# Kernel optimization log

Hardware: AMD Instinct MI355X
Metric: run time of the kernel (lower is better)

## Reference

```python
import jax, jax.numpy as jnp
import numpy as np

THRESHOLD = 1.0


def heaviside(x):
    return (x > 0).astype(x.dtype)


def lif_parallel(x, W_ih, b_ih, b_hh, beta):
    """snntorch LeakyParallel: RNN with relu nonlinearity and diagonal
    recurrent weight = beta, followed by threshold spike (no reset).
    x: [T, B, I]; W_ih: [H, I]; beta: [H]. Returns spikes [T, B, H]."""
    beta = jnp.clip(beta, 0.0, 1.0)
    # input projection is time-parallel (one big GEMM)
    z = jnp.einsum('tbi,hi->tbh', x, W_ih) + b_ih + b_hh  # [T, B, H]

    def step(h, z_t):
        h_new = jax.nn.relu(z_t + beta * h)
        return h_new, h_new

    h0 = jnp.zeros(z.shape[1:], z.dtype)
    _, mem = jax.lax.scan(step, h0, z)  # [T, B, H]
    return heaviside(mem - THRESHOLD)


def setup_inputs() -> dict:
    key = jax.random.key(0)
    ks = jax.random.split(key, 9)
    T, B, I, H, O = 200, 256, 784, 1000, 10
    s1 = 1.0 / np.sqrt(I)
    s2 = 1.0 / np.sqrt(H)
    return {
        'x': jax.random.normal(ks[0], (T, B, I), dtype=jnp.float32),
        'W_ih1': jax.random.normal(ks[1], (H, I), dtype=jnp.float32) * s1,
        'b_ih1': jax.random.normal(ks[2], (H,), dtype=jnp.float32) * s1,
        'b_hh1': jax.random.normal(ks[3], (H,), dtype=jnp.float32) * s1,
        'beta1': jnp.full((H,), 0.95, dtype=jnp.float32),
        'W_ih2': jax.random.normal(ks[4], (O, H), dtype=jnp.float32) * s2,
        'b_ih2': jax.random.normal(ks[5], (O,), dtype=jnp.float32) * s2,
        'b_hh2': jax.random.normal(ks[6], (O,), dtype=jnp.float32) * s2,
        'beta2': jnp.full((O,), 0.95, dtype=jnp.float32),
    }


def reference(x, W_ih1, b_ih1, b_hh1, beta1, W_ih2, b_ih2, b_hh2, beta2):
    spk1 = lif_parallel(x, W_ih1, b_ih1, b_hh1, beta1)   # [T, B, 1000]
    spk2 = lif_parallel(spk1, W_ih2, b_ih2, b_hh2, beta2)  # [T, B, 10]
    return spk2
```

## Files before the change

kernel.cpp:

```cpp
#include <hip/hip_runtime.h>
#include <cstdint>
#include <cstddef>

#define T_STEPS 200
#define B_SZ    256
#define I_SZ    784
#define H_SZ    1000
#define O_SZ    10
#define M_ROWS  (T_STEPS * B_SZ)

#define KT        25
#define TILE_WORDS 4096
#define MBLKS     400
#define NBLKS     8

__device__ __forceinline__ int swz32(int g) { return (g & 24) | ((g + (g >> 3)) & 7); }
__device__ __forceinline__ int inv32(int p) { return (p & 24) | ((p - (p >> 3)) & 7); }

typedef const __attribute__((address_space(1))) void gvoid;
typedef __attribute__((address_space(3))) void lvoid;
__device__ __forceinline__ void gload16(const void* g, void* l) {
    __builtin_amdgcn_global_load_lds((gvoid*)g, (lvoid*)l, 16, 0, 0);
}

__global__ __launch_bounds__(256) void pack_kernel(
    const float* __restrict__ src, float* __restrict__ dst, int nrows)
{
    int bid = blockIdx.x;
    int blk = bid / KT, kt = bid - blk * KT;

    __shared__ float T[32 * 132];
    const int tid = threadIdx.x;

    #pragma unroll
    for (int it = 0; it < 4; ++it) {
        int id = tid + it * 256;
        int r  = id >> 3;
        int c4 = id & 7;
        int row = blk * 128 + r;
        int k   = kt * 32 + c4 * 4;
        float4 v = make_float4(0.f, 0.f, 0.f, 0.f);
        if (row < nrows && k < I_SZ)
            v = *(const float4*)(src + (size_t)row * I_SZ + k);
        T[(c4*4 + 0) * 132 + r] = v.x;
        T[(c4*4 + 1) * 132 + r] = v.y;
        T[(c4*4 + 2) * 132 + r] = v.z;
        T[(c4*4 + 3) * 132 + r] = v.w;
    }
    __syncthreads();

    float* out = dst + (size_t)(blk * KT + kt) * TILE_WORDS;
    #pragma unroll
    for (int it = 0; it < 4; ++it) {
        int id = tid + it * 256;
        int k  = id >> 5;
        int pg = id & 31;
        int g  = inv32(pg);
        float4 v = *(const float4*)&T[k * 132 + g * 4];
        *(float4*)(out + k * 128 + pg * 4) = v;
    }
}

__global__ __launch_bounds__(256, 4) void gemm1_v3(
    const float* __restrict__ Xp, const float* __restrict__ Wp,
    const float* __restrict__ b_ih, const float* __restrict__ b_hh,
    float* __restrict__ Z)
{
    __shared__ float Al[TILE_WORDS];
    __shared__ float Bl[TILE_WORDS];

    const int tid = threadIdx.x;
    const int tr  = tid >> 4;
    const int tc  = tid & 15;

    int bid  = blockIdx.x;
    int wg   = (bid & 7) * 400 + (bid >> 3);
    int mblk = wg >> 3;
    int nblk = wg & 7;
    const int row0 = mblk * 128;
    const int col0 = nblk * 128;

    const int a0 = swz32(2*tr)     * 4;
    const int a1 = swz32(2*tr + 1) * 4;
    const int b0 = swz32(2*tc)     * 4;
    const int b1 = swz32(2*tc + 1) * 4;

    const float* pA = Xp + (size_t)mblk * KT * TILE_WORDS;
    const float* pB = Wp + (size_t)nblk * KT * TILE_WORDS;

    float acc[8][8] = {};

    for (int kt = 0; kt < KT; ++kt) {
        const float* sA = pA + kt * TILE_WORDS + tid * 4;
        const float* sB = pB + kt * TILE_WORDS + tid * 4;
        gload16(sA,        &Al[        tid * 4]);
        gload16(sA + 1024, &Al[1024 + tid * 4]);
        gload16(sA + 2048, &Al[2048 + tid * 4]);
        gload16(sA + 3072, &Al[3072 + tid * 4]);
        gload16(sB,        &Bl[        tid * 4]);
        gload16(sB + 1024, &Bl[1024 + tid * 4]);
        gload16(sB + 2048, &Bl[2048 + tid * 4]);
        gload16(sB + 3072, &Bl[3072 + tid * 4]);
        __syncthreads();

        #pragma unroll 2
        for (int k = 0; k < 32; ++k) {
            const int kb = k * 128;
            float4 A0 = *(const float4*)&Al[kb + a0];
            float4 A1 = *(const float4*)&Al[kb + a1];
            float4 B0 = *(const float4*)&Bl[kb + b0];
            float4 B1 = *(const float4*)&Bl[kb + b1];
            float a[8] = {A0.x, A0.y, A0.z, A0.w, A1.x, A1.y, A1.z, A1.w};
            float b[8] = {B0.x, B0.y, B0.z, B0.w, B1.x, B1.y, B1.z, B1.w};
            #pragma unroll
            for (int i = 0; i < 8; ++i)
                #pragma unroll
                for (int j = 0; j < 8; ++j)
                    acc[i][j] = fmaf(a[i], b[j], acc[i][j]);
        }
        __syncthreads();
    }

    float bias[8];
    #pragma unroll
    for (int j = 0; j < 8; ++j) {
        int cc = col0 + tc * 8 + j;
        bias[j] = (cc < H_SZ) ? (b_ih[cc] + b_hh[cc]) : 0.f;
    }

    const bool full = (col0 + 127 < H_SZ);
    #pragma unroll
    for (int i = 0; i < 8; ++i) {
        int rr = row0 + tr * 8 + i;
        float* zrow = Z + (size_t)rr * H_SZ + col0 + tc * 8;
        if (full) {
            float4 v0 = make_float4(acc[i][0] + bias[0], acc[i][1] + bias[1],
                                    acc[i][2] + bias[2], acc[i][3] + bias[3]);
            float4 v1 = make_float4(acc[i][4] + bias[4], acc[i][5] + bias[5],
                                    acc[i][6] + bias[6], acc[i][7] + bias[7]);
            *(float4*)(zrow + 0) = v0;
            *(float4*)(zrow + 4) = v1;
        } else {
            #pragma unroll
            for (int j = 0; j < 8; ++j) {
                int cc = col0 + tc * 8 + j;
                if (cc < H_SZ) zrow[j] = acc[i][j] + bias[j];
            }
        }
    }
}

__global__ __launch_bounds__(256) void scan1_kernel(
    float* __restrict__ Z, const float* __restrict__ beta)
{
    int idx = blockIdx.x * blockDim.x + threadIdx.x;
    if (idx >= B_SZ * H_SZ) return;
    int h = idx % H_SZ;
    float be = fminf(fmaxf(beta[h], 0.f), 1.f);
    float hm = 0.f;
    const size_t stride = (size_t)B_SZ * H_SZ;
    float* p = Z + idx;
    for (int t = 0; t < T_STEPS; ++t) {
        float v = p[(size_t)t * stride];
        hm = fmaxf(fmaf(be, hm, v), 0.f);
        p[(size_t)t * stride] = (hm > 1.0f) ? 1.0f : 0.0f;
    }
}

__global__ __launch_bounds__(256) void gemm2_kernel(
    const float* __restrict__ S, const float* __restrict__ W2,
    const float* __restrict__ b_ih2, const float* __restrict__ b_hh2,
    float* __restrict__ Z2)
{
    __shared__ float W2s[O_SZ * H_SZ];
    for (int i = threadIdx.x; i < O_SZ * H_SZ; i += blockDim.x)
        W2s[i] = W2[i];
    __syncthreads();

    const int wave  = threadIdx.x >> 6;
    const int lane  = threadIdx.x & 63;
    const int wgid  = blockIdx.x * (blockDim.x >> 6) + wave;
    const int nwave = gridDim.x * (blockDim.x >> 6);

    for (int m = wgid; m < M_ROWS; m += nwave) {
        const float* row = S + (size_t)m * H_SZ;
        float acc[O_SZ];
        #pragma unroll
        for (int o = 0; o < O_SZ; ++o) acc[o] = 0.f;

        for (int h = lane; h < H_SZ; h += 64) {
            float s = row[h];
            #pragma unroll
            for (int o = 0; o < O_SZ; ++o)
                acc[o] = fmaf(s, W2s[o * H_SZ + h], acc[o]);
        }
        #pragma unroll
        for (int o = 0; o < O_SZ; ++o) {
            float v = acc[o];
            #pragma unroll
            for (int off = 32; off > 0; off >>= 1)
                v += __shfl_down(v, off, 64);
            if (lane == 0)
                Z2[(size_t)m * O_SZ + o] = v + b_ih2[o] + b_hh2[o];
        }
    }
}

#define CH 20
__global__ __launch_bounds__(256) void scan2_kernel(
    float* __restrict__ Z2io, const float* __restrict__ beta2)
{
    int idx = blockIdx.x * blockDim.x + threadIdx.x;
    if (idx >= B_SZ * O_SZ) return;
    int o = idx % O_SZ;
    float be = fminf(fmaxf(beta2[o], 0.f), 1.f);
    float hm = 0.f;
    const int stride = B_SZ * O_SZ;
    for (int t0 = 0; t0 < T_STEPS; t0 += CH) {
        float v[CH];
        #pragma unroll
        for (int i = 0; i < CH; ++i)
            v[i] = Z2io[(size_t)(t0 + i) * stride + idx];
        #pragma unroll
        for (int i = 0; i < CH; ++i) {
            hm = fmaxf(fmaf(be, hm, v[i]), 0.f);
            Z2io[(size_t)(t0 + i) * stride + idx] = (hm > 1.0f) ? 1.0f : 0.0f;
        }
    }
}

extern "C" void kernel_launch(void* const* d_in, const int* in_sizes, int n_in,
                              void* d_out, int out_size, void* d_ws, size_t ws_size,
                              hipStream_t stream)
{
    const float* x     = (const float*)d_in[0];
    const float* W1    = (const float*)d_in[1];
    const float* bih1  = (const float*)d_in[2];
    const float* bhh1  = (const float*)d_in[3];
    const float* beta1 = (const float*)d_in[4];
    const float* W2    = (const float*)d_in[5];
    const float* bih2  = (const float*)d_in[6];
    const float* bhh2  = (const float*)d_in[7];
    const float* beta2 = (const float*)d_in[8];
    float* out = (float*)d_out;

    char* base = (char*)d_ws;
    float* z1 = (float*)base;
    float* Xp = (float*)(base + (size_t)M_ROWS * H_SZ * 4);
    float* Wp = Xp + (size_t)MBLKS * KT * TILE_WORDS;

    pack_kernel<<<MBLKS * KT, 256, 0, stream>>>(x,  Xp, M_ROWS);
    pack_kernel<<<NBLKS * KT, 256, 0, stream>>>(W1, Wp, H_SZ);

    gemm1_v3<<<MBLKS * NBLKS, 256, 0, stream>>>(Xp, Wp, bih1, bhh1, z1);

    scan1_kernel<<<(B_SZ * H_SZ) / 256, 256, 0, stream>>>(z1, beta1);
    gemm2_kernel<<<2048, 256, 0, stream>>>(z1, W2, bih2, bhh2, out);
    scan2_kernel<<<(B_SZ * O_SZ + 255) / 256, 256, 0, stream>>>(out, beta2);
}
```

Before: 1.184 ms.

## Double-buffer LDS tiles in GEMM1 to overlap global loads with FMAs

GEMM1 now uses two LDS buffers per operand. The next K-tile is issued via global_load_lds before computing on the current one, leaving one barrier per iteration instead of two. The inner K loop is fully unrolled, and launch bounds drop from 4 to 2 blocks per CU, trading occupancy for latency hiding and more registers. There is a correctness risk: the async LDS loads for the next tile are not explicitly waited on before the barrier that precedes their use. Whether the compiler's vmcnt handling covers this is unclear.

Result: slower. 1.267 ms (+7.0%).

```diff
diff --git a/kernel.cpp b/kernel.cpp
--- a/kernel.cpp
+++ b/kernel.cpp
@@ -61,13 +61,13 @@
     }
 }
 
-__global__ __launch_bounds__(256, 4) void gemm1_v3(
+__global__ __launch_bounds__(256, 2) void gemm1_v4(
     const float* __restrict__ Xp, const float* __restrict__ Wp,
     const float* __restrict__ b_ih, const float* __restrict__ b_hh,
     float* __restrict__ Z)
 {
-    __shared__ float Al[TILE_WORDS];
-    __shared__ float Bl[TILE_WORDS];
+    __shared__ float Al[2][TILE_WORDS];
+    __shared__ float Bl[2][TILE_WORDS];
 
     const int tid = threadIdx.x;
     const int tr  = tid >> 4;
@@ -90,33 +90,47 @@
 
     float acc[8][8] = {};
 
-    for (int kt = 0; kt < KT; ++kt) {
+    auto stage = [&](int kt, int b) {
         const float* sA = pA + kt * TILE_WORDS + tid * 4;
         const float* sB = pB + kt * TILE_WORDS + tid * 4;
-        gload16(sA,        &Al[        tid * 4]);
-        gload16(sA + 1024, &Al[1024 + tid * 4]);
-        gload16(sA + 2048, &Al[2048 + tid * 4]);
-        gload16(sA + 3072, &Al[3072 + tid * 4]);
-        gload16(sB,        &Bl[        tid * 4]);
-        gload16(sB + 1024, &Bl[1024 + tid * 4]);
-        gload16(sB + 2048, &Bl[2048 + tid * 4]);
-        gload16(sB + 3072, &Bl[3072 + tid * 4]);
-        __syncthreads();
-
-        #pragma unroll 2
+        gload16(sA,        &Al[b][        tid * 4]);
+        gload16(sA + 1024, &Al[b][1024 + tid * 4]);
+        gload16(sA + 2048, &Al[b][2048 + tid * 4]);
+        gload16(sA + 3072, &Al[b][3072 + tid * 4]);
+        gload16(sB,        &Bl[b][        tid * 4]);
+        gload16(sB + 1024, &Bl[b][1024 + tid * 4]);
+        gload16(sB + 2048, &Bl[b][2048 + tid * 4]);
+        gload16(sB + 3072, &Bl[b][3072 + tid * 4]);
+    };
+
+    stage(0, 0);
+    __syncthreads();
+
+    for (int kt = 0; kt < KT; ++kt) {
+        const int cur = kt & 1;
+        if (kt + 1 < KT) stage(kt + 1, cur ^ 1);
+
+        const float* A = Al[cur];
+        const float* B = Bl[cur];
+
+        #pragma unroll
         for (int k = 0; k < 32; ++k) {
-            const int kb = k * 128;
-            float4 A0 = *(const float4*)&Al[kb + a0];
-            float4 A1 = *(const float4*)&Al[kb + a1];
-            float4 B0 = *(const float4*)&Bl[kb + b0];
-            float4 B1 = *(const float4*)&Bl[kb + b1];
-            float a[8] = {A0.x, A0.y, A0.z, A0.w, A1.x, A1.y, A1.z, A1.w};
-            float b[8] = {B0.x, B0.y, B0.z, B0.w, B1.x, B1.y, B1.z, B1.w};
-            #pragma unroll
-            for (int i = 0; i < 8; ++i)
-                #pragma unroll
-                for (int j = 0; j < 8; ++j)
-                    acc[i][j] = fmaf(a[i], b[j], acc[i][j]);
+            const float4 A0 = *(const float4*)&A[k*128 + a0];
+            const float4 A1 = *(const float4*)&A[k*128 + a1];
+            const float4 B0 = *(const float4*)&B[k*128 + b0];
+            const float4 B1 = *(const float4*)&B[k*128 + b1];
+            #define FMA_ROW(i, av) \
+                acc[i][0] = fmaf(av, B0.x, acc[i][0]); \
+                acc[i][1] = fmaf(av, B0.y, acc[i][1]); \
+                acc[i][2] = fmaf(av, B0.z, acc[i][2]); \
+                acc[i][3] = fmaf(av, B0.w, acc[i][3]); \
+                acc[i][4] = fmaf(av, B1.x, acc[i][4]); \
+                acc[i][5] = fmaf(av, B1.y, acc[i][5]); \
+                acc[i][6] = fmaf(av, B1.z, acc[i][6]); \
+                acc[i][7] = fmaf(av, B1.w, acc[i][7]);
+            FMA_ROW(0, A0.x) FMA_ROW(1, A0.y) FMA_ROW(2, A0.z) FMA_ROW(3, A0.w)
+            FMA_ROW(4, A1.x) FMA_ROW(5, A1.y) FMA_ROW(6, A1.z) FMA_ROW(7, A1.w)
+            #undef FMA_ROW
         }
         __syncthreads();
     }
@@ -252,7 +266,7 @@
     pack_kernel<<<MBLKS * KT, 256, 0, stream>>>(x,  Xp, M_ROWS);
     pack_kernel<<<NBLKS * KT, 256, 0, stream>>>(W1, Wp, H_SZ);
 
-    gemm1_v3<<<MBLKS * NBLKS, 256, 0, stream>>>(Xp, Wp, bih1, bhh1, z1);
+    gemm1_v4<<<MBLKS * NBLKS, 256, 0, stream>>>(Xp, Wp, bih1, bhh1, z1);
 
     scan1_kernel<<<(B_SZ * H_SZ) / 256, 256, 0, stream>>>(z1, beta1);
     gemm2_kernel<<<2048, 256, 0, stream>>>(z1, W2, bih2, bhh2, out);
```
